# Kernel tuning notes

Hardware: AMD Instinct MI355X
Metric: run time of the kernel (lower is better)

The kernel has to match this reference:

```python
import math
import jax, jax.numpy as jnp
import numpy as np

H = 8  # num_heads

def _layernorm(x, scale, bias, eps=1e-5):
    m = x.mean(-1, keepdims=True)
    v = x.var(-1, keepdims=True)
    return (x - m) / jnp.sqrt(v + eps) * scale + bias

def setup_inputs() -> dict:
    key = jax.random.key(0)
    ks = jax.random.split(key, 12)
    B, C, P, D, G = 8, 32, 256, 256, 512
    n = jax.random.normal
    return {
        "qz": n(ks[0], (B, C, P, D), dtype=jnp.float32),
        "unary": n(ks[1], (B, C, P, D), dtype=jnp.float32),
        # per-sample condition-instantiated factors; scaled ~1/sqrt(D) so attn logits are sane
        "time_u": n(ks[2], (B, D, D), dtype=jnp.float32) * 0.06,
        "time_v": n(ks[3], (B, D, D), dtype=jnp.float32) * 0.06,
        "channel_u": n(ks[4], (B, D, D), dtype=jnp.float32) * 0.06,
        "channel_v": n(ks[5], (B, D, D), dtype=jnp.float32) * 0.06,
        "topic_binary": n(ks[6], (B, G, D), dtype=jnp.float32) * 0.02,
        "norm_scale": jnp.ones((D,), jnp.float32),
        "norm_bias": jnp.zeros((D,), jnp.float32),
        "gate_w": n(ks[7], (D, D), dtype=jnp.float32) * 0.02,
        "gate_b": jnp.zeros((D,), jnp.float32),
        "out_w1": n(ks[8], (D, D), dtype=jnp.float32) * 0.02,
        "out_b1": jnp.zeros((D,), jnp.float32),
        "out_w2": n(ks[9], (D, D), dtype=jnp.float32) * 0.02,
        "out_b2": jnp.zeros((D,), jnp.float32),
    }

def reference(qz, unary, time_u, time_v, channel_u, channel_v, topic_binary,
              norm_scale, norm_bias, gate_w, gate_b, out_w1, out_b1, out_w2, out_b2):
    B, C, P, D = qz.shape
    R = D // H
    inv_sqrt_r = 1.0 / math.sqrt(R)

    qz_n = _layernorm(qz, norm_scale, norm_bias)

    def heads(x, w):  # [B,C,P,D] x [B,D,D] -> [B,C,P,H,R]
        return jnp.einsum('bcpd,bod->bcpo', x, w).reshape(B, C, P, H, R)

    # --- time-factor message: attention over P within each (b, c, h) ---
    qu = heads(qz_n, time_u).transpose(0, 1, 3, 2, 4)   # [B,C,H,P,R]
    qv = heads(qz_n, time_v).transpose(0, 1, 3, 2, 4)
    attn_t = jax.nn.softmax(jnp.einsum('bchpr,bchqr->bchpq', qu, qv) * inv_sqrt_r, axis=-1)
    m_t = jnp.einsum('bchpq,bcqd->bchpd', attn_t, qz_n).mean(axis=2)  # [B,C,P,D]

    # --- channel-factor message: attention over C within each (b, p, h) ---
    qu = heads(qz_n, channel_u).transpose(0, 2, 3, 1, 4)  # [B,P,H,C,R]
    qv = heads(qz_n, channel_v).transpose(0, 2, 3, 1, 4)
    attn_c = jax.nn.softmax(jnp.einsum('bphcr,bphfr->bphcf', qu, qv) * inv_sqrt_r, axis=-1)
    qzp = qz_n.transpose(0, 2, 1, 3)                      # [B,P,C,D]
    m_c = jnp.einsum('bphcf,bpfd->bphcd', attn_c, qzp).mean(axis=2).transpose(0, 2, 1, 3)

    # --- topic-modeling binary factor with AbsNormalize (relu + L1-normalize) ---
    qg = jax.nn.relu(jnp.einsum('bcpd,bgd->bcpg', qz_n, topic_binary))
    qg = qg / jnp.maximum(qg.sum(axis=-1, keepdims=True), 1e-6)
    m_g = jnp.einsum('bcpg,bgd->bcpd', qg, topic_binary)

    # --- gated residual update ---
    gate = jax.nn.sigmoid(qz @ gate_w.T + gate_b)
    qz2 = gate * qz + (1.0 - gate) * (unary + m_t + m_c + m_g)

    # --- output MLP with shared LayerNorm ---
    h = _layernorm(qz2, norm_scale, norm_bias)
    h = jax.nn.gelu(h @ out_w1.T + out_b1, approximate=False) @ out_w2.T + out_b2
    return qz2 + h
```

## Files before the change

### kernel.cpp

```cpp
#include <hip/hip_runtime.h>
#include <math.h>

namespace {

constexpr float INV_SQRT_R = 0.17677669529663689f;

typedef __attribute__((ext_vector_type(8))) __bf16 bf16x8;
typedef __attribute__((ext_vector_type(4))) float f32x4;

static __device__ __forceinline__ f32x4 MF(bf16x8 a, bf16x8 b, f32x4 c) {
    return __builtin_amdgcn_mfma_f32_16x16x32_bf16(a, b, c, 0, 0, 0);
}

__global__ __launch_bounds__(256) void cvt_kernel(
    const float* __restrict__ src, __bf16* __restrict__ dst, int n)
{
    int i = (blockIdx.x * 256 + threadIdx.x) * 4;
    if (i < n) {
        float4 v = *(const float4*)(src + i);
        dst[i + 0] = (__bf16)v.x; dst[i + 1] = (__bf16)v.y;
        dst[i + 2] = (__bf16)v.z; dst[i + 3] = (__bf16)v.w;
    }
}

__global__ __launch_bounds__(256) void cvt2_kernel(
    const float* __restrict__ src, __bf16* __restrict__ dst, int n,
    int dstChunk, int dstOff)
{
    int i = (blockIdx.x * 256 + threadIdx.x) * 4;
    if (i < n) {
        float4 v = *(const float4*)(src + i);
        int o = (i >> 16) * dstChunk + dstOff + (i & 65535);
        dst[o + 0] = (__bf16)v.x; dst[o + 1] = (__bf16)v.y;
        dst[o + 2] = (__bf16)v.z; dst[o + 3] = (__bf16)v.w;
    }
}

__global__ __launch_bounds__(256) void ln_kernel(
    const float* __restrict__ x, const float* __restrict__ sc,
    const float* __restrict__ bi, __bf16* __restrict__ y)
{
    const size_t row = blockIdx.x;
    const int t = threadIdx.x;
    const float v = x[row * 256 + t];
    float s = v, s2 = v * v;
    #pragma unroll
    for (int o = 32; o > 0; o >>= 1) {
        s  += __shfl_xor(s, o);
        s2 += __shfl_xor(s2, o);
    }
    __shared__ float ps[4], ps2[4];
    if ((t & 63) == 0) { ps[t >> 6] = s; ps2[t >> 6] = s2; }
    __syncthreads();
    const float S  = ps[0] + ps[1] + ps[2] + ps[3];
    const float S2 = ps2[0] + ps2[1] + ps2[2] + ps2[3];
    const float mean = S * (1.0f / 256.0f);
    const float var  = S2 * (1.0f / 256.0f) - mean * mean;
    const float inv  = 1.0f / sqrtf(var + 1e-5f);
    y[row * 256 + t] = (__bf16)((v - mean) * inv * sc[t] + bi[t]);
}

__global__ __launch_bounds__(256) void tpose_bf_kernel(
    const __bf16* __restrict__ src, __bf16* __restrict__ dst, int R, int C)
{
    const size_t bz = blockIdx.z;
    src += bz * (size_t)R * C;
    dst += bz * (size_t)R * C;
    __shared__ __bf16 tile[32][34];
    const int r0 = blockIdx.x * 32, c0 = blockIdx.y * 32;
    const int tx = threadIdx.x & 31, ty = threadIdx.x >> 5;
    #pragma unroll
    for (int i = 0; i < 32; i += 8)
        tile[ty + i][tx] = src[(size_t)(r0 + ty + i) * C + c0 + tx];
    __syncthreads();
    #pragma unroll
    for (int i = 0; i < 32; i += 8)
        dst[(size_t)(c0 + ty + i) * R + r0 + tx] = tile[tx][ty + i];
}

__global__ __launch_bounds__(256) void tpose_cvt_kernel(
    const float* __restrict__ src, __bf16* __restrict__ dst, int R, int C)
{
    const size_t bz = blockIdx.z;
    src += bz * (size_t)R * C;
    dst += bz * (size_t)R * C;
    __shared__ __bf16 tile[32][34];
    const int r0 = blockIdx.x * 32, c0 = blockIdx.y * 32;
    const int tx = threadIdx.x & 31, ty = threadIdx.x >> 5;
    #pragma unroll
    for (int i = 0; i < 32; i += 8)
        tile[ty + i][tx] = (__bf16)src[(size_t)(r0 + ty + i) * C + c0 + tx];
    __syncthreads();
    #pragma unroll
    for (int i = 0; i < 32; i += 8)
        dst[(size_t)(c0 + ty + i) * R + r0 + tx] = tile[tx][ty + i];
}

__global__ __launch_bounds__(256) void mgemm_kernel(
    const __bf16* __restrict__ A, const __bf16* __restrict__ Bm, __bf16* __restrict__ Cout,
    int K, size_t aStride, size_t bStride,
    size_t s_b, size_t s_c, size_t s_p, size_t s_w, size_t s_h)
{
    const int bb = blockIdx.z;
    const int m0 = blockIdx.x * 64;
    const int n0 = blockIdx.y * 256;
    const __bf16* Ab = A + (size_t)bb * aStride;
    const __bf16* Bb = Bm + (size_t)bb * bStride;
    __shared__ __align__(16) __bf16 As[64][40];
    __shared__ __align__(16) __bf16 Bs[256][40];
    const int t = threadIdx.x;
    const int lane = t & 63;
    const int wid = t >> 6;
    const int l15 = lane & 15, lg = lane >> 4;

    f32x4 acc[4][4] = {};

    for (int k0 = 0; k0 < K; k0 += 32) {
        {
            const int row = t >> 2, k8 = (t & 3) << 3;
            *(bf16x8*)&As[row][k8] = *(const bf16x8*)(Ab + (size_t)(m0 + row) * K + k0 + k8);
        }
        #pragma unroll
        for (int s = 0; s < 4; ++s) {
            const int slot = s * 256 + t;
            const int row = slot >> 2, k8 = (slot & 3) << 3;
            *(bf16x8*)&Bs[row][k8] = *(const bf16x8*)(Bb + (size_t)(n0 + row) * K + k0 + k8);
        }
        __syncthreads();
        bf16x8 af[4], bfr[4];
        #pragma unroll
        for (int i = 0; i < 4; ++i)
            af[i] = *(const bf16x8*)&As[i * 16 + l15][lg * 8];
        #pragma unroll
        for (int j = 0; j < 4; ++j)
            bfr[j] = *(const bf16x8*)&Bs[wid * 64 + j * 16 + l15][lg * 8];
        #pragma unroll
        for (int i = 0; i < 4; ++i)
            #pragma unroll
            for (int j = 0; j < 4; ++j)
                acc[i][j] = MF(af[i], bfr[j], acc[i][j]);
        __syncthreads();
    }

    #pragma unroll
    for (int j = 0; j < 4; ++j) {
        const int n = n0 + wid * 64 + j * 16 + l15;
        const size_t offn = (size_t)(n >> 8) * s_w + (size_t)((n >> 5) & 7) * s_h + (n & 31);
        #pragma unroll
        for (int i = 0; i < 4; ++i) {
            #pragma unroll
            for (int r = 0; r < 4; ++r) {
                const int m = m0 + i * 16 + lg * 4 + r;
                const size_t off = (size_t)bb * s_b + (size_t)(m >> 8) * s_c
                                 + (size_t)(m & 255) * s_p + offn;
                Cout[off] = (__bf16)acc[i][j][r];
            }
        }
    }
}

__global__ __launch_bounds__(256) void time_attn_mt_kernel(
    const __bf16* __restrict__ qu, const __bf16* __restrict__ qv,
    const __bf16* __restrict__ qznT, __bf16* __restrict__ m_t)
{
    const int bc = blockIdx.x;
    const int p0 = blockIdx.y * 64;
    const __bf16* quB = qu + (size_t)bc * 65536;
    const __bf16* qvB = qv + (size_t)bc * 65536;
    const __bf16* BT  = qznT + (size_t)bc * 65536;
    __shared__ __align__(16) __bf16 R1[27136];
    __bf16* Us  = R1;
    __bf16* Vs  = R1 + 2560;
    __bf16* aL  = R1;
    __bf16* Bs2 = R1 + 16896;
    const int t = threadIdx.x;
    const int lane = t & 63;
    const int wid = t >> 6;
    const int l15 = lane & 15, lg = lane >> 4;

    f32x4 acc[16] = {};

    for (int h = 0; h < 8; ++h) {
        const __bf16* quH = quB + h * 8192;
        const __bf16* qvH = qvB + h * 8192;
        __syncthreads();
        {
            const int row = t >> 2, k8 = (t & 3) << 3;
            *(bf16x8*)&Us[row * 40 + k8] = *(const bf16x8*)(quH + (size_t)(p0 + row) * 32 + k8);
        }
        #pragma unroll
        for (int i = 0; i < 4; ++i) {
            const int slot = i * 256 + t;
            const int row = slot >> 2, k8 = (slot & 3) << 3;
            *(bf16x8*)&Vs[row * 40 + k8] = *(const bf16x8*)(qvH + (size_t)row * 32 + k8);
        }
        __syncthreads();

        f32x4 s[16];
        bf16x8 a = *(const bf16x8*)&Us[(wid * 16 + l15) * 40 + lg * 8];
        #pragma unroll
        for (int j = 0; j < 16; ++j) {
            bf16x8 bfr = *(const bf16x8*)&Vs[(j * 16 + l15) * 40 + lg * 8];
            s[j] = MF(a, bfr, (f32x4){0.f, 0.f, 0.f, 0.f});
        }

        #pragma unroll
        for (int r = 0; r < 4; ++r) {
            float e[16];
            float sum = 0.0f;
            #pragma unroll
            for (int j = 0; j < 16; ++j) {
                e[j] = __expf(s[j][r] * INV_SQRT_R);
                sum += e[j];
            }
            sum += __shfl_xor(sum, 1);
            sum += __shfl_xor(sum, 2);
            sum += __shfl_xor(sum, 4);
            sum += __shfl_xor(sum, 8);
            const float inv = 0.125f / sum;
            #pragma unroll
            for (int j = 0; j < 16; ++j) acc[j][r] += e[j] * inv;
        }
    }

    __syncthreads();
    #pragma unroll
    for (int r = 0; r < 4; ++r) {
        const int row = wid * 16 + lg * 4 + r;
        #pragma unroll
        for (int j = 0; j < 16; ++j)
            aL[row * 264 + j * 16 + l15] = (__bf16)acc[j][r];
    }
    __syncthreads();

    f32x4 acc2[4][4] = {};
    for (int k0 = 0; k0 < 256; k0 += 32) {
        #pragma unroll
        for (int s = 0; s < 4; ++s) {
            const int slot = s * 256 + t;
            const int row = slot >> 2, k8 = (slot & 3) << 3;
            *(bf16x8*)&Bs2[row * 40 + k8] = *(const bf16x8*)(BT + (size_t)row * 256 + k0 + k8);
        }
        __syncthreads();
        bf16x8 af[4], bfr[4];
        #pragma unroll
        for (int i = 0; i < 4; ++i)
            af[i] = *(const bf16x8*)&aL[(i * 16 + l15) * 264 + k0 + lg * 8];
        #pragma unroll
        for (int j = 0; j < 4; ++j)
            bfr[j] = *(const bf16x8*)&Bs2[(wid * 64 + j * 16 + l15) * 40 + lg * 8];
        #pragma unroll
        for (int i = 0; i < 4; ++i)
            #pragma unroll
            for (int j = 0; j < 4; ++j)
                acc2[i][j] = MF(af[i], bfr[j], acc2[i][j]);
        __syncthreads();
    }
    #pragma unroll
    for (int i = 0; i < 4; ++i)
        #pragma unroll
        for (int j = 0; j < 4; ++j) {
            const int d = wid * 64 + j * 16 + l15;
            #pragma unroll
            for (int r = 0; r < 4; ++r) {
                const int p = p0 + i * 16 + lg * 4 + r;
                m_t[(size_t)bc * 65536 + (size_t)p * 256 + d] = (__bf16)acc2[i][j][r];
            }
        }
}

__global__ __launch_bounds__(256) void chan_fused_kernel(
    const __bf16* __restrict__ quc, const __bf16* __restrict__ qvc,
    const __bf16* __restrict__ qzn, __bf16* __restrict__ m_c)
{
    const int bp = blockIdx.x;
    const int b = bp >> 8, p = bp & 255;
    const __bf16* quB = quc + (size_t)bp * 8192;
    const __bf16* qvB = qvc + (size_t)bp * 8192;
    __shared__ __align__(16) __bf16 QU[20480];
    __shared__ float ab[32 * 33];
    __bf16* qus = QU;
    __bf16* qvs = QU + 10240;
    const int t = threadIdx.x;
    #pragma unroll
    for (int i = 0; i < 4; ++i) {
        int fi = i * 256 + t;
        int e = fi << 3;
        int h = e >> 10, cc = (e >> 5) & 31, r = e & 31;
        int base = (h * 32 + cc) * 40 + r;
        *(bf16x8*)&qus[base] = *(const bf16x8*)(quB + e);
        *(bf16x8*)&qvs[base] = *(const bf16x8*)(qvB + e);
    }
    __syncthreads();
    const int c = t >> 3, j = t & 7;
    float acc[4] = {0.f, 0.f, 0.f, 0.f};
    for (int h = 0; h < 8; ++h) {
        float qur[32];
        #pragma unroll
        for (int u = 0; u < 4; ++u) {
            bf16x8 q8 = *(const bf16x8*)&qus[(h * 32 + c) * 40 + u * 8];
            #pragma unroll
            for (int e2 = 0; e2 < 8; ++e2) qur[u * 8 + e2] = (float)q8[e2];
        }
        float s[4];
        #pragma unroll
        for (int jj = 0; jj < 4; ++jj) {
            int f = j * 4 + jj;
            float a = 0.f;
            #pragma unroll
            for (int u = 0; u < 4; ++u) {
                bf16x8 v8 = *(const bf16x8*)&qvs[(h * 32 + f) * 40 + u * 8];
                #pragma unroll
                for (int e2 = 0; e2 < 8; ++e2) a += qur[u * 8 + e2] * (float)v8[e2];
            }
            s[jj] = a * INV_SQRT_R;
        }
        float mx = fmaxf(fmaxf(s[0], s[1]), fmaxf(s[2], s[3]));
        mx = fmaxf(mx, __shfl_xor(mx, 1));
        mx = fmaxf(mx, __shfl_xor(mx, 2));
        mx = fmaxf(mx, __shfl_xor(mx, 4));
        float e0x = __expf(s[0] - mx), e1x = __expf(s[1] - mx);
        float e2x = __expf(s[2] - mx), e3x = __expf(s[3] - mx);
        float sum = e0x + e1x + e2x + e3x;
        sum += __shfl_xor(sum, 1);
        sum += __shfl_xor(sum, 2);
        sum += __shfl_xor(sum, 4);
        float inv = 0.125f / sum;
        acc[0] += e0x * inv; acc[1] += e1x * inv; acc[2] += e2x * inv; acc[3] += e3x * inv;
    }
    #pragma unroll
    for (int jj = 0; jj < 4; ++jj) ab[c * 33 + j * 4 + jj] = acc[jj];
    __syncthreads();
    float* bt = (float*)QU;
    #pragma unroll 4
    for (int f = 0; f < 32; ++f)
        bt[f * 256 + t] = (float)qzn[((size_t)(b * 32 + f) * 256 + p) * 256 + t];
    __syncthreads();
    for (int c2 = 0; c2 < 32; c2 += 2) {
        float a0 = 0.f, a1 = 0.f;
        #pragma unroll
        for (int f = 0; f < 32; ++f) {
            float v = bt[f * 256 + t];
            a0 += ab[c2 * 33 + f] * v;
            a1 += ab[(c2 + 1) * 33 + f] * v;
        }
        size_t off = ((size_t)(b * 32 + c2) * 256 + p) * 256 + t;
        m_c[off] = (__bf16)a0;
        m_c[off + 65536] = (__bf16)a1;
    }
}

__global__ __launch_bounds__(256, 2) void topic_fused_kernel(
    const __bf16* __restrict__ qzn, const __bf16* __restrict__ topicb,
    const __bf16* __restrict__ topicTb, __bf16* __restrict__ m_g)
{
    const int bb = blockIdx.z;
    const int m0 = blockIdx.x * 32;
    const __bf16* Ab = qzn + (size_t)bb * 2097152;
    const __bf16* B1 = topicb + (size_t)bb * 131072;
    const __bf16* B2 = topicTb + (size_t)bb * 131072;
    __shared__ __align__(16) __bf16 As[32][40];
    __shared__ __align__(16) __bf16 Bs[512][40];
    __shared__ __align__(16) __bf16 Ps[32][520];
    __shared__ float rsInv[32];
    const int t = threadIdx.x;
    const int lane = t & 63, wid = t >> 6;
    const int l15 = lane & 15, lg = lane >> 4;

    f32x4 acc[2][8] = {};
    for (int k0 = 0; k0 < 256; k0 += 32) {
        if (t < 128) {
            const int row = t >> 2, k8 = (t & 3) << 3;
            *(bf16x8*)&As[row][k8] = *(const bf16x8*)(Ab + (size_t)(m0 + row) * 256 + k0 + k8);
        }
        #pragma unroll
        for (int s = 0; s < 8; ++s) {
            const int slot = s * 256 + t;
            const int row = slot >> 2, k8 = (slot & 3) << 3;
            *(bf16x8*)&Bs[row][k8] = *(const bf16x8*)(B1 + (size_t)row * 256 + k0 + k8);
        }
        __syncthreads();
        bf16x8 af0 = *(const bf16x8*)&As[l15][lg * 8];
        bf16x8 af1 = *(const bf16x8*)&As[16 + l15][lg * 8];
        #pragma unroll
        for (int j = 0; j < 8; ++j) {
            bf16x8 b8 = *(const bf16x8*)&Bs[wid * 128 + j * 16 + l15][lg * 8];
            acc[0][j] = MF(af0, b8, acc[0][j]);
            acc[1][j] = MF(af1, b8, acc[1][j]);
        }
        __syncthreads();
    }
    #pragma unroll
    for (int i = 0; i < 2; ++i)
        #pragma unroll
        for (int j = 0; j < 8; ++j) {
            const int n = wid * 128 + j * 16 + l15;
            #pragma unroll
            for (int r = 0; r < 4; ++r)
                Ps[i * 16 + lg * 4 + r][n] = (__bf16)fmaxf(acc[i][j][r], 0.0f);
        }
    __syncthreads();
    {
        const int row = t >> 3, seg = t & 7;
        float s = 0.0f;
        #pragma unroll
        for (int u = 0; u < 8; ++u) {
            bf16x8 v = *(const bf16x8*)&Ps[row][seg * 64 + u * 8];
            #pragma unroll
            for (int e = 0; e < 8; ++e) s += (float)v[e];
        }
        s += __shfl_xor(s, 1);
        s += __shfl_xor(s, 2);
        s += __shfl_xor(s, 4);
        if (seg == 0) rsInv[row] = 1.0f / fmaxf(s, 1e-6f);
    }
    __syncthreads();
    f32x4 acc2[2][4] = {};
    for (int k0 = 0; k0 < 512; k0 += 32) {
        #pragma unroll
        for (int s = 0; s < 4; ++s) {
            const int slot = s * 256 + t;
            const int row = slot >> 2, k8 = (slot & 3) << 3;
            *(bf16x8*)&Bs[row][k8] = *(const bf16x8*)(B2 + (size_t)row * 512 + k0 + k8);
        }
        __syncthreads();
        bf16x8 af0 = *(const bf16x8*)&Ps[l15][k0 + lg * 8];
        bf16x8 af1 = *(const bf16x8*)&Ps[16 + l15][k0 + lg * 8];
        #pragma unroll
        for (int j = 0; j < 4; ++j) {
            bf16x8 b8 = *(const bf16x8*)&Bs[wid * 64 + j * 16 + l15][lg * 8];
            acc2[0][j] = MF(af0, b8, acc2[0][j]);
            acc2[1][j] = MF(af1, b8, acc2[1][j]);
        }
        __syncthreads();
    }
    #pragma unroll
    for (int i = 0; i < 2; ++i)
        #pragma unroll
        for (int j = 0; j < 4; ++j) {
            const int n = wid * 64 + j * 16 + l15;
            #pragma unroll
            for (int r = 0; r < 4; ++r) {
                const int ml = i * 16 + lg * 4 + r;
                m_g[(size_t)bb * 2097152 + (size_t)(m0 + ml) * 256 + n]
                    = (__bf16)(acc2[i][j][r] * rsInv[ml]);
            }
        }
}

__global__ __launch_bounds__(256, 2) void mega_kernel(
    const float* __restrict__ qz, const float* __restrict__ unary,
    const __bf16* __restrict__ m_t, const __bf16* __restrict__ m_c,
    const __bf16* __restrict__ m_g,
    const __bf16* __restrict__ gwb, const float* __restrict__ gate_b,
    const __bf16* __restrict__ w1b, const float* __restrict__ b1,
    const __bf16* __restrict__ w2b, const float* __restrict__ b2,
    const float* __restrict__ nsc, const float* __restrict__ nbi,
    float* __restrict__ outp)
{
    const int m0 = blockIdx.x * 64;
    __shared__ __align__(16) __bf16 Bs[256][40];
    __shared__ __align__(16) __bf16 hL[64][264];
    __shared__ float lnp[64][4][2];
    const int t = threadIdx.x;
    const int lane = t & 63, wid = t >> 6;
    const int l15 = lane & 15, lg = lane >> 4;

    #pragma unroll
    for (int s = 0; s < 8; ++s) {
        const int slot = s * 256 + t;
        const int row = slot >> 5;
        const int k8 = (slot & 31) << 3;
        const float* src = qz + (size_t)(m0 + row) * 256 + k8;
        float4 v0 = *(const float4*)src;
        float4 v1 = *(const float4*)(src + 4);
        bf16x8 pk;
        pk[0] = (__bf16)v0.x; pk[1] = (__bf16)v0.y; pk[2] = (__bf16)v0.z; pk[3] = (__bf16)v0.w;
        pk[4] = (__bf16)v1.x; pk[5] = (__bf16)v1.y; pk[6] = (__bf16)v1.z; pk[7] = (__bf16)v1.w;
        *(bf16x8*)&hL[row][k8] = pk;
    }

    f32x4 acc[4][4] = {};
    for (int k0 = 0; k0 < 256; k0 += 32) {
        #pragma unroll
        for (int s = 0; s < 4; ++s) {
            const int slot = s * 256 + t;
            const int row = slot >> 2, k8 = (slot & 3) << 3;
            *(bf16x8*)&Bs[row][k8] = *(const bf16x8*)(gwb + (size_t)row * 256 + k0 + k8);
        }
        __syncthreads();
        bf16x8 af[4], bfr[4];
        #pragma unroll
        for (int i = 0; i < 4; ++i) af[i] = *(const bf16x8*)&hL[i * 16 + l15][k0 + lg * 8];
        #pragma unroll
        for (int j = 0; j < 4; ++j) bfr[j] = *(const bf16x8*)&Bs[wid * 64 + j * 16 + l15][lg * 8];
        #pragma unroll
        for (int i = 0; i < 4; ++i)
            #pragma unroll
            for (int j = 0; j < 4; ++j)
                acc[i][j] = MF(af[i], bfr[j], acc[i][j]);
        __syncthreads();
    }

    f32x4 z2[4][4];
    #pragma unroll
    for (int i = 0; i < 4; ++i) {
        #pragma unroll
        for (int r = 0; r < 4; ++r) {
            const int rr = i * 16 + lg * 4 + r;
            float s = 0.0f, s2 = 0.0f;
            #pragma unroll
            for (int j = 0; j < 4; ++j) {
                const int n = wid * 64 + j * 16 + l15;
                const size_t off = (size_t)(m0 + rr) * 256 + n;
                float g = 1.0f / (1.0f + __expf(-(acc[i][j][r] + gate_b[n])));
                float rest = unary[off] + (float)m_t[off] + (float)m_c[off] + (float)m_g[off];
                float v = g * (float)hL[rr][n] + (1.0f - g) * rest;
                z2[i][j][r] = v;
                s += v; s2 += v * v;
            }
            s  += __shfl_xor(s, 1);  s  += __shfl_xor(s, 2);
            s  += __shfl_xor(s, 4);  s  += __shfl_xor(s, 8);
            s2 += __shfl_xor(s2, 1); s2 += __shfl_xor(s2, 2);
            s2 += __shfl_xor(s2, 4); s2 += __shfl_xor(s2, 8);
            if (l15 == 0) {
                lnp[rr][wid][0] = s;
                lnp[rr][wid][1] = s2;
            }
        }
    }
    __syncthreads();
    #pragma unroll
    for (int i = 0; i < 4; ++i) {
        #pragma unroll
        for (int r = 0; r < 4; ++r) {
            const int rr = i * 16 + lg * 4 + r;
            float S  = lnp[rr][0][0] + lnp[rr][1][0] + lnp[rr][2][0] + lnp[rr][3][0];
            float S2 = lnp[rr][0][1] + lnp[rr][1][1] + lnp[rr][2][1] + lnp[rr][3][1];
            float mean = S * (1.0f / 256.0f);
            float var  = S2 * (1.0f / 256.0f) - mean * mean;
            float inv  = 1.0f / sqrtf(var + 1e-5f);
            #pragma unroll
            for (int j = 0; j < 4; ++j) {
                const int n = wid * 64 + j * 16 + l15;
                hL[rr][n] = (__bf16)((z2[i][j][r] - mean) * inv * nsc[n] + nbi[n]);
            }
        }
    }
    __syncthreads();

    f32x4 acc2[4][4] = {};
    for (int k0 = 0; k0 < 256; k0 += 32) {
        #pragma unroll
        for (int s = 0; s < 4; ++s) {
            const int slot = s * 256 + t;
            const int row = slot >> 2, k8 = (slot & 3) << 3;
            *(bf16x8*)&Bs[row][k8] = *(const bf16x8*)(w1b + (size_t)row * 256 + k0 + k8);
        }
        __syncthreads();
        bf16x8 af[4], bfr[4];
        #pragma unroll
        for (int i = 0; i < 4; ++i) af[i] = *(const bf16x8*)&hL[i * 16 + l15][k0 + lg * 8];
        #pragma unroll
        for (int j = 0; j < 4; ++j) bfr[j] = *(const bf16x8*)&Bs[wid * 64 + j * 16 + l15][lg * 8];
        #pragma unroll
        for (int i = 0; i < 4; ++i)
            #pragma unroll
            for (int j = 0; j < 4; ++j)
                acc2[i][j] = MF(af[i], bfr[j], acc2[i][j]);
        __syncthreads();
    }
    #pragma unroll
    for (int i = 0; i < 4; ++i)
        #pragma unroll
        for (int j = 0; j < 4; ++j) {
            const int n = wid * 64 + j * 16 + l15;
            const float bn = b1[n];
            #pragma unroll
            for (int r = 0; r < 4; ++r) {
                float x = acc2[i][j][r] + bn;
                hL[i * 16 + lg * 4 + r][n] = (__bf16)(0.5f * x * (1.0f + erff(x * 0.7071067811865475f)));
            }
        }
    __syncthreads();

    f32x4 acc3[4][4] = {};
    for (int k0 = 0; k0 < 256; k0 += 32) {
        #pragma unroll
        for (int s = 0; s < 4; ++s) {
            const int slot = s * 256 + t;
            const int row = slot >> 2, k8 = (slot & 3) << 3;
            *(bf16x8*)&Bs[row][k8] = *(const bf16x8*)(w2b + (size_t)row * 256 + k0 + k8);
        }
        __syncthreads();
        bf16x8 af[4], bfr[4];
        #pragma unroll
        for (int i = 0; i < 4; ++i) af[i] = *(const bf16x8*)&hL[i * 16 + l15][k0 + lg * 8];
        #pragma unroll
        for (int j = 0; j < 4; ++j) bfr[j] = *(const bf16x8*)&Bs[wid * 64 + j * 16 + l15][lg * 8];
        #pragma unroll
        for (int i = 0; i < 4; ++i)
            #pragma unroll
            for (int j = 0; j < 4; ++j)
                acc3[i][j] = MF(af[i], bfr[j], acc3[i][j]);
        __syncthreads();
    }
    #pragma unroll
    for (int i = 0; i < 4; ++i)
        #pragma unroll
        for (int j = 0; j < 4; ++j) {
            const int n = wid * 64 + j * 16 + l15;
            const float bn = b2[n];
            #pragma unroll
            for (int r = 0; r < 4; ++r) {
                const size_t off = (size_t)(m0 + i * 16 + lg * 4 + r) * 256 + n;
                outp[off] = z2[i][j][r] + acc3[i][j][r] + bn;
            }
        }
}

}

extern "C" void kernel_launch(void* const* d_in, const int* in_sizes, int n_in,
                              void* d_out, int out_size, void* d_ws, size_t ws_size,
                              hipStream_t stream)
{
    (void)in_sizes; (void)n_in; (void)out_size; (void)ws_size;
    const float* qz     = (const float*)d_in[0];
    const float* unary  = (const float*)d_in[1];
    const float* time_u = (const float*)d_in[2];
    const float* time_v = (const float*)d_in[3];
    const float* chan_u = (const float*)d_in[4];
    const float* chan_v = (const float*)d_in[5];
    const float* topic  = (const float*)d_in[6];
    const float* nsc    = (const float*)d_in[7];
    const float* nbi    = (const float*)d_in[8];
    const float* gate_w = (const float*)d_in[9];
    const float* gate_b = (const float*)d_in[10];
    const float* w1     = (const float*)d_in[11];
    const float* b1     = (const float*)d_in[12];
    const float* w2     = (const float*)d_in[13];
    const float* b2     = (const float*)d_in[14];

    char* base = (char*)d_ws;
    __bf16* qzn_b  = (__bf16*)base;
    __bf16* pool   = (__bf16*)(base + (32ull << 20));
    __bf16* wtime  = pool;
    __bf16* wchan  = pool + 1048576;
    __bf16* topicb = pool + 2097152;
    __bf16* topicTb= pool + 3145728;
    __bf16* gwb    = pool + 4194304;
    __bf16* w1b    = pool + 4259840;
    __bf16* w2b    = pool + 4325376;
    __bf16* Blo    = (__bf16*)(base + (64ull << 20));
    __bf16* Bhi    = (__bf16*)(base + (96ull << 20));
    __bf16* qu_t   = Blo;
    __bf16* qv_t   = Bhi;
    __bf16* qu_c   = Blo;
    __bf16* qv_c   = Bhi;
    __bf16* m_g    = Blo;
    __bf16* qznT   = (__bf16*)(base + (128ull << 20));
    __bf16* m_c    = qznT;
    __bf16* m_t    = (__bf16*)(base + (160ull << 20));
    float*  OUTF   = (float*)d_out;

    dim3 blk(256);

    cvt2_kernel<<<512, blk, 0, stream>>>(time_u, wtime, 524288, 131072, 0);
    cvt2_kernel<<<512, blk, 0, stream>>>(time_v, wtime, 524288, 131072, 65536);
    cvt2_kernel<<<512, blk, 0, stream>>>(chan_u, wchan, 524288, 131072, 0);
    cvt2_kernel<<<512, blk, 0, stream>>>(chan_v, wchan, 524288, 131072, 65536);
    cvt_kernel<<<1024, blk, 0, stream>>>(topic, topicb, 1048576);
    tpose_cvt_kernel<<<dim3(16, 8, 8), blk, 0, stream>>>(topic, topicTb, 512, 256);
    cvt_kernel<<<64, blk, 0, stream>>>(gate_w, gwb, 65536);
    cvt_kernel<<<64, blk, 0, stream>>>(w1, w1b, 65536);
    cvt_kernel<<<64, blk, 0, stream>>>(w2, w2b, 65536);

    ln_kernel<<<65536, blk, 0, stream>>>(qz, nsc, nbi, qzn_b);
    tpose_bf_kernel<<<dim3(8, 8, 256), blk, 0, stream>>>(qzn_b, qznT, 256, 256);

    mgemm_kernel<<<dim3(128, 2, 8), blk, 0, stream>>>(
        qzn_b, wtime, qu_t, 256, 2097152, 131072,
        2097152, 65536, 32, 16777216, 8192);

    time_attn_mt_kernel<<<dim3(256, 4), blk, 0, stream>>>(qu_t, qv_t, qznT, m_t);

    mgemm_kernel<<<dim3(128, 2, 8), blk, 0, stream>>>(
        qzn_b, wchan, qu_c, 256, 2097152, 131072,
        2097152, 32, 8192, 16777216, 1024);

    chan_fused_kernel<<<2048, blk, 0, stream>>>(qu_c, qv_c, qzn_b, m_c);

    topic_fused_kernel<<<dim3(256, 1, 8), blk, 0, stream>>>(qzn_b, topicb, topicTb, m_g);

    mega_kernel<<<1024, blk, 0, stream>>>(
        qz, unary, m_t, m_c, m_g,
        gwb, gate_b, w1b, b1, w2b, b2, nsc, nbi, OUTF);
}
```

Baseline: 540.7 us.

## Load GEMM B operands directly from global memory, drop LDS staging and syncs

Across the projection GEMM, time attention, topic and mega kernels, the B-operand (weights / transposed activations) is now read straight from global memory into MFMA fragments instead of being staged through shared memory every K-step. The A tile is loaded into LDS once for the full K, which removes the per-iteration barriers. The smaller LDS footprint allows higher occupancy hints in launch_bounds. The cost is more uncoalesced-ish 16-byte global loads that depend on L1/L2 reuse, since B rows are re-read by every block.

```diff
diff --git a/kernel.cpp b/kernel.cpp
--- a/kernel.cpp
+++ b/kernel.cpp
@@ -96,50 +96,45 @@
         dst[(size_t)(c0 + ty + i) * R + r0 + tx] = tile[tx][ty + i];
 }
 
-__global__ __launch_bounds__(256) void mgemm_kernel(
+__global__ __launch_bounds__(256, 4) void mgemm_kernel(
     const __bf16* __restrict__ A, const __bf16* __restrict__ Bm, __bf16* __restrict__ Cout,
-    int K, size_t aStride, size_t bStride,
+    size_t aStride, size_t bStride,
     size_t s_b, size_t s_c, size_t s_p, size_t s_w, size_t s_h)
 {
     const int bb = blockIdx.z;
     const int m0 = blockIdx.x * 64;
     const int n0 = blockIdx.y * 256;
     const __bf16* Ab = A + (size_t)bb * aStride;
-    const __bf16* Bb = Bm + (size_t)bb * bStride;
-    __shared__ __align__(16) __bf16 As[64][40];
-    __shared__ __align__(16) __bf16 Bs[256][40];
+    const __bf16* Bb = Bm + (size_t)bb * bStride + (size_t)n0 * 256;
+    __shared__ __align__(16) __bf16 As[64][264];
     const int t = threadIdx.x;
     const int lane = t & 63;
     const int wid = t >> 6;
     const int l15 = lane & 15, lg = lane >> 4;
 
+    #pragma unroll
+    for (int s = 0; s < 8; ++s) {
+        const int slot = s * 256 + t;
+        const int row = slot >> 5, k8 = (slot & 31) << 3;
+        *(bf16x8*)&As[row][k8] = *(const bf16x8*)(Ab + (size_t)(m0 + row) * 256 + k8);
+    }
+    __syncthreads();
+
     f32x4 acc[4][4] = {};
-
-    for (int k0 = 0; k0 < K; k0 += 32) {
-        {
-            const int row = t >> 2, k8 = (t & 3) << 3;
-            *(bf16x8*)&As[row][k8] = *(const bf16x8*)(Ab + (size_t)(m0 + row) * K + k0 + k8);
-        }
-        #pragma unroll
-        for (int s = 0; s < 4; ++s) {
-            const int slot = s * 256 + t;
-            const int row = slot >> 2, k8 = (slot & 3) << 3;
-            *(bf16x8*)&Bs[row][k8] = *(const bf16x8*)(Bb + (size_t)(n0 + row) * K + k0 + k8);
-        }
-        __syncthreads();
+    #pragma unroll
+    for (int k0 = 0; k0 < 256; k0 += 32) {
         bf16x8 af[4], bfr[4];
         #pragma unroll
         for (int i = 0; i < 4; ++i)
-            af[i] = *(const bf16x8*)&As[i * 16 + l15][lg * 8];
+            af[i] = *(const bf16x8*)&As[i * 16 + l15][k0 + lg * 8];
         #pragma unroll
         for (int j = 0; j < 4; ++j)
-            bfr[j] = *(const bf16x8*)&Bs[wid * 64 + j * 16 + l15][lg * 8];
+            bfr[j] = *(const bf16x8*)(Bb + (size_t)(wid * 64 + j * 16 + l15) * 256 + k0 + lg * 8);
         #pragma unroll
         for (int i = 0; i < 4; ++i)
             #pragma unroll
             for (int j = 0; j < 4; ++j)
                 acc[i][j] = MF(af[i], bfr[j], acc[i][j]);
-        __syncthreads();
     }
 
     #pragma unroll
@@ -159,7 +154,7 @@
     }
 }
 
-__global__ __launch_bounds__(256) void time_attn_mt_kernel(
+__global__ __launch_bounds__(256, 3) void time_attn_mt_kernel(
     const __bf16* __restrict__ qu, const __bf16* __restrict__ qv,
     const __bf16* __restrict__ qznT, __bf16* __restrict__ m_t)
 {
@@ -168,11 +163,10 @@
     const __bf16* quB = qu + (size_t)bc * 65536;
     const __bf16* qvB = qv + (size_t)bc * 65536;
     const __bf16* BT  = qznT + (size_t)bc * 65536;
-    __shared__ __align__(16) __bf16 R1[27136];
+    __shared__ __align__(16) __bf16 R1[16896];
     __bf16* Us  = R1;
     __bf16* Vs  = R1 + 2560;
     __bf16* aL  = R1;
-    __bf16* Bs2 = R1 + 16896;
     const int t = threadIdx.x;
     const int lane = t & 63;
     const int wid = t >> 6;
@@ -234,27 +228,20 @@
     __syncthreads();
 
     f32x4 acc2[4][4] = {};
+    #pragma unroll
     for (int k0 = 0; k0 < 256; k0 += 32) {
-        #pragma unroll
-        for (int s = 0; s < 4; ++s) {
-            const int slot = s * 256 + t;
-            const int row = slot >> 2, k8 = (slot & 3) << 3;
-            *(bf16x8*)&Bs2[row * 40 + k8] = *(const bf16x8*)(BT + (size_t)row * 256 + k0 + k8);
-        }
-        __syncthreads();
         bf16x8 af[4], bfr[4];
         #pragma unroll
         for (int i = 0; i < 4; ++i)
             af[i] = *(const bf16x8*)&aL[(i * 16 + l15) * 264 + k0 + lg * 8];
         #pragma unroll
         for (int j = 0; j < 4; ++j)
-            bfr[j] = *(const bf16x8*)&Bs2[(wid * 64 + j * 16 + l15) * 40 + lg * 8];
+            bfr[j] = *(const bf16x8*)(BT + (size_t)(wid * 64 + j * 16 + l15) * 256 + k0 + lg * 8);
         #pragma unroll
         for (int i = 0; i < 4; ++i)
             #pragma unroll
             for (int j = 0; j < 4; ++j)
                 acc2[i][j] = MF(af[i], bfr[j], acc2[i][j]);
-        __syncthreads();
     }
     #pragma unroll
     for (int i = 0; i < 4; ++i)
@@ -350,7 +337,7 @@
     }
 }
 
-__global__ __launch_bounds__(256, 2) void topic_fused_kernel(
+__global__ __launch_bounds__(256, 3) void topic_fused_kernel(
     const __bf16* __restrict__ qzn, const __bf16* __restrict__ topicb,
     const __bf16* __restrict__ topicTb, __bf16* __restrict__ m_g)
 {
@@ -359,36 +346,32 @@
     const __bf16* Ab = qzn + (size_t)bb * 2097152;
     const __bf16* B1 = topicb + (size_t)bb * 131072;
     const __bf16* B2 = topicTb + (size_t)bb * 131072;
-    __shared__ __align__(16) __bf16 As[32][40];
-    __shared__ __align__(16) __bf16 Bs[512][40];
+    __shared__ __align__(16) __bf16 As[32][264];
     __shared__ __align__(16) __bf16 Ps[32][520];
     __shared__ float rsInv[32];
     const int t = threadIdx.x;
     const int lane = t & 63, wid = t >> 6;
     const int l15 = lane & 15, lg = lane >> 4;
 
+    #pragma unroll
+    for (int s = 0; s < 4; ++s) {
+        const int slot = s * 256 + t;
+        const int row = slot >> 5, k8 = (slot & 31) << 3;
+        *(bf16x8*)&As[row][k8] = *(const bf16x8*)(Ab + (size_t)(m0 + row) * 256 + k8);
+    }
+    __syncthreads();
+
     f32x4 acc[2][8] = {};
+    #pragma unroll
     for (int k0 = 0; k0 < 256; k0 += 32) {
-        if (t < 128) {
-            const int row = t >> 2, k8 = (t & 3) << 3;
-            *(bf16x8*)&As[row][k8] = *(const bf16x8*)(Ab + (size_t)(m0 + row) * 256 + k0 + k8);
-        }
-        #pragma unroll
-        for (int s = 0; s < 8; ++s) {
-            const int slot = s * 256 + t;
-            const int row = slot >> 2, k8 = (slot & 3) << 3;
-            *(bf16x8*)&Bs[row][k8] = *(const bf16x8*)(B1 + (size_t)row * 256 + k0 + k8);
-        }
-        __syncthreads();
-        bf16x8 af0 = *(const bf16x8*)&As[l15][lg * 8];
-        bf16x8 af1 = *(const bf16x8*)&As[16 + l15][lg * 8];
+        bf16x8 af0 = *(const bf16x8*)&As[l15][k0 + lg * 8];
+        bf16x8 af1 = *(const bf16x8*)&As[16 + l15][k0 + lg * 8];
         #pragma unroll
         for (int j = 0; j < 8; ++j) {
-            bf16x8 b8 = *(const bf16x8*)&Bs[wid * 128 + j * 16 + l15][lg * 8];
+            bf16x8 b8 = *(const bf16x8*)(B1 + (size_t)(wid * 128 + j * 16 + l15) * 256 + k0 + lg * 8);
             acc[0][j] = MF(af0, b8, acc[0][j]);
             acc[1][j] = MF(af1, b8, acc[1][j]);
         }
-        __syncthreads();
     }
     #pragma unroll
     for (int i = 0; i < 2; ++i)
@@ -416,23 +399,16 @@
     }
     __syncthreads();
     f32x4 acc2[2][4] = {};
+    #pragma unroll
     for (int k0 = 0; k0 < 512; k0 += 32) {
-        #pragma unroll
-        for (int s = 0; s < 4; ++s) {
-            const int slot = s * 256 + t;
-            const int row = slot >> 2, k8 = (slot & 3) << 3;
-            *(bf16x8*)&Bs[row][k8] = *(const bf16x8*)(B2 + (size_t)row * 512 + k0 + k8);
-        }
-        __syncthreads();
         bf16x8 af0 = *(const bf16x8*)&Ps[l15][k0 + lg * 8];
         bf16x8 af1 = *(const bf16x8*)&Ps[16 + l15][k0 + lg * 8];
         #pragma unroll
         for (int j = 0; j < 4; ++j) {
-            bf16x8 b8 = *(const bf16x8*)&Bs[wid * 64 + j * 16 + l15][lg * 8];
+            bf16x8 b8 = *(const bf16x8*)(B2 + (size_t)(wid * 64 + j * 16 + l15) * 512 + k0 + lg * 8);
             acc2[0][j] = MF(af0, b8, acc2[0][j]);
             acc2[1][j] = MF(af1, b8, acc2[1][j]);
         }
-        __syncthreads();
     }
     #pragma unroll
     for (int i = 0; i < 2; ++i)
@@ -448,7 +424,7 @@
         }
 }
 
-__global__ __launch_bounds__(256, 2) void mega_kernel(
+__global__ __launch_bounds__(256, 3) void mega_kernel(
     const float* __restrict__ qz, const float* __restrict__ unary,
     const __bf16* __restrict__ m_t, const __bf16* __restrict__ m_c,
     const __bf16* __restrict__ m_g,
@@ -459,7 +435,6 @@
     float* __restrict__ outp)
 {
     const int m0 = blockIdx.x * 64;
-    __shared__ __align__(16) __bf16 Bs[256][40];
     __shared__ __align__(16) __bf16 hL[64][264];
     __shared__ float lnp[64][4][2];
     const int t = threadIdx.x;
@@ -479,27 +454,22 @@
         pk[4] = (__bf16)v1.x; pk[5] = (__bf16)v1.y; pk[6] = (__bf16)v1.z; pk[7] = (__bf16)v1.w;
         *(bf16x8*)&hL[row][k8] = pk;
     }
+    __syncthreads();
 
     f32x4 acc[4][4] = {};
+    #pragma unroll
     for (int k0 = 0; k0 < 256; k0 += 32) {
-        #pragma unroll
-        for (int s = 0; s < 4; ++s) {
-            const int slot = s * 256 + t;
-            const int row = slot >> 2, k8 = (slot & 3) << 3;
-            *(bf16x8*)&Bs[row][k8] = *(const bf16x8*)(gwb + (size_t)row * 256 + k0 + k8);
-        }
-        __syncthreads();
         bf16x8 af[4], bfr[4];
         #pragma unroll
         for (int i = 0; i < 4; ++i) af[i] = *(const bf16x8*)&hL[i * 16 + l15][k0 + lg * 8];
         #pragma unroll
-        for (int j = 0; j < 4; ++j) bfr[j] = *(const bf16x8*)&Bs[wid * 64 + j * 16 + l15][lg * 8];
+        for (int j = 0; j < 4; ++j)
+            bfr[j] = *(const bf16x8*)(gwb + (size_t)(wid * 64 + j * 16 + l15) * 256 + k0 + lg * 8);
         #pragma unroll
         for (int i = 0; i < 4; ++i)
             #pragma unroll
             for (int j = 0; j < 4; ++j)
                 acc[i][j] = MF(af[i], bfr[j], acc[i][j]);
-        __syncthreads();
     }
 
     f32x4 z2[4][4];
@@ -550,26 +520,21 @@
     __syncthreads();
 
     f32x4 acc2[4][4] = {};
+    #pragma unroll
     for (int k0 = 0; k0 < 256; k0 += 32) {
-        #pragma unroll
-        for (int s = 0; s < 4; ++s) {
-            const int slot = s * 256 + t;
-            const int row = slot >> 2, k8 = (slot & 3) << 3;
-            *(bf16x8*)&Bs[row][k8] = *(const bf16x8*)(w1b + (size_t)row * 256 + k0 + k8);
-        }
-        __syncthreads();
         bf16x8 af[4], bfr[4];
         #pragma unroll
         for (int i = 0; i < 4; ++i) af[i] = *(const bf16x8*)&hL[i * 16 + l15][k0 + lg * 8];
         #pragma unroll
-        for (int j = 0; j < 4; ++j) bfr[j] = *(const bf16x8*)&Bs[wid * 64 + j * 16 + l15][lg * 8];
+        for (int j = 0; j < 4; ++j)
+            bfr[j] = *(const bf16x8*)(w1b + (size_t)(wid * 64 + j * 16 + l15) * 256 + k0 + lg * 8);
         #pragma unroll
         for (int i = 0; i < 4; ++i)
             #pragma unroll
             for (int j = 0; j < 4; ++j)
                 acc2[i][j] = MF(af[i], bfr[j], acc2[i][j]);
-        __syncthreads();
-    }
+    }
+    __syncthreads();
     #pragma unroll
     for (int i = 0; i < 4; ++i)
         #pragma unroll
@@ -585,25 +550,19 @@
     __syncthreads();
 
     f32x4 acc3[4][4] = {};
+    #pragma unroll
     for (int k0 = 0; k0 < 256; k0 += 32) {
-        #pragma unroll
-        for (int s = 0; s < 4; ++s) {
-            const int slot = s * 256 + t;
-            const int row = slot >> 2, k8 = (slot & 3) << 3;
-            *(bf16x8*)&Bs[row][k8] = *(const bf16x8*)(w2b + (size_t)row * 256 + k0 + k8);
-        }
-        __syncthreads();
         bf16x8 af[4], bfr[4];
         #pragma unroll
         for (int i = 0; i < 4; ++i) af[i] = *(const bf16x8*)&hL[i * 16 + l15][k0 + lg * 8];
         #pragma unroll
-        for (int j = 0; j < 4; ++j) bfr[j] = *(const bf16x8*)&Bs[wid * 64 + j * 16 + l15][lg * 8];
+        for (int j = 0; j < 4; ++j)
+            bfr[j] = *(const bf16x8*)(w2b + (size_t)(wid * 64 + j * 16 + l15) * 256 + k0 + lg * 8);
         #pragma unroll
         for (int i = 0; i < 4; ++i)
             #pragma unroll
             for (int j = 0; j < 4; ++j)
                 acc3[i][j] = MF(af[i], bfr[j], acc3[i][j]);
-        __syncthreads();
     }
     #pragma unroll
     for (int i = 0; i < 4; ++i)
@@ -680,13 +639,13 @@
     tpose_bf_kernel<<<dim3(8, 8, 256), blk, 0, stream>>>(qzn_b, qznT, 256, 256);
 
     mgemm_kernel<<<dim3(128, 2, 8), blk, 0, stream>>>(
-        qzn_b, wtime, qu_t, 256, 2097152, 131072,
+        qzn_b, wtime, qu_t, 2097152, 131072,
         2097152, 65536, 32, 16777216, 8192);
 
     time_attn_mt_kernel<<<dim3(256, 4), blk, 0, stream>>>(qu_t, qv_t, qznT, m_t);
 
     mgemm_kernel<<<dim3(128, 2, 8), blk, 0, stream>>>(
-        qzn_b, wchan, qu_c, 256, 2097152, 131072,
+        qzn_b, wchan, qu_c, 2097152, 131072,
         2097152, 32, 8192, 16777216, 1024);
 
     chan_fused_kernel<<<2048, blk, 0, stream>>>(qu_c, qv_c, qzn_b, m_c);
```

Result: slower. 639.3 us (+18.2%).

## Remap block indices so batch varies fastest across XCDs, raise occupancy

Applied to the files above, without the earlier changes.

Flattens grids for the GEMM, time-attention, channel and topic kernels and remaps block ids so consecutive blocks map to different batch/bc groups. Given MI355X's round-robin dispatch of workgroups across XCDs, the intent appears to be keeping each batch's weights and data in one XCD's L2. The channel kernel now preloads its qzn column into registers before the attention phase instead of staging it through shared memory, removing a barrier and LDS traffic. The mega kernel reuses the Bs buffer for its LayerNorm partial sums to save LDS, and it and the channel kernel get occupancy hints of 3 blocks per CU, which risks register spills.

```diff
diff --git a/kernel.cpp b/kernel.cpp
--- a/kernel.cpp
+++ b/kernel.cpp
@@ -101,9 +101,11 @@
     int K, size_t aStride, size_t bStride,
     size_t s_b, size_t s_c, size_t s_p, size_t s_w, size_t s_h)
 {
-    const int bb = blockIdx.z;
-    const int m0 = blockIdx.x * 64;
-    const int n0 = blockIdx.y * 256;
+    const int bid = blockIdx.x;
+    const int bb = bid & 7;
+    const int rest = bid >> 3;
+    const int n0 = (rest & 1) * 256;
+    const int m0 = (rest >> 1) * 64;
     const __bf16* Ab = A + (size_t)bb * aStride;
     const __bf16* Bb = Bm + (size_t)bb * bStride;
     __shared__ __align__(16) __bf16 As[64][40];
@@ -163,8 +165,10 @@
     const __bf16* __restrict__ qu, const __bf16* __restrict__ qv,
     const __bf16* __restrict__ qznT, __bf16* __restrict__ m_t)
 {
-    const int bc = blockIdx.x;
-    const int p0 = blockIdx.y * 64;
+    const int bid = blockIdx.x;
+    const int jj0 = bid >> 3;
+    const int bc = (bid & 7) * 32 + (jj0 >> 2);
+    const int p0 = (jj0 & 3) * 64;
     const __bf16* quB = qu + (size_t)bc * 65536;
     const __bf16* qvB = qv + (size_t)bc * 65536;
     const __bf16* BT  = qznT + (size_t)bc * 65536;
@@ -269,12 +273,13 @@
         }
 }
 
-__global__ __launch_bounds__(256) void chan_fused_kernel(
+__global__ __launch_bounds__(256, 3) void chan_fused_kernel(
     const __bf16* __restrict__ quc, const __bf16* __restrict__ qvc,
     const __bf16* __restrict__ qzn, __bf16* __restrict__ m_c)
 {
-    const int bp = blockIdx.x;
-    const int b = bp >> 8, p = bp & 255;
+    const int bid = blockIdx.x;
+    const int b = bid & 7, p = bid >> 3;
+    const int bp = b * 256 + p;
     const __bf16* quB = quc + (size_t)bp * 8192;
     const __bf16* qvB = qvc + (size_t)bp * 8192;
     __shared__ __align__(16) __bf16 QU[20480];
@@ -282,6 +287,12 @@
     __bf16* qus = QU;
     __bf16* qvs = QU + 10240;
     const int t = threadIdx.x;
+
+    float btr[32];
+    #pragma unroll
+    for (int f = 0; f < 32; ++f)
+        btr[f] = (float)qzn[((size_t)(b * 32 + f) * 256 + p) * 256 + t];
+
     #pragma unroll
     for (int i = 0; i < 4; ++i) {
         int fi = i * 256 + t;
@@ -331,16 +342,12 @@
     #pragma unroll
     for (int jj = 0; jj < 4; ++jj) ab[c * 33 + j * 4 + jj] = acc[jj];
     __syncthreads();
-    float* bt = (float*)QU;
-    #pragma unroll 4
-    for (int f = 0; f < 32; ++f)
-        bt[f * 256 + t] = (float)qzn[((size_t)(b * 32 + f) * 256 + p) * 256 + t];
-    __syncthreads();
+    #pragma unroll 2
     for (int c2 = 0; c2 < 32; c2 += 2) {
         float a0 = 0.f, a1 = 0.f;
         #pragma unroll
         for (int f = 0; f < 32; ++f) {
-            float v = bt[f * 256 + t];
+            float v = btr[f];
             a0 += ab[c2 * 33 + f] * v;
             a1 += ab[(c2 + 1) * 33 + f] * v;
         }
@@ -354,8 +361,9 @@
     const __bf16* __restrict__ qzn, const __bf16* __restrict__ topicb,
     const __bf16* __restrict__ topicTb, __bf16* __restrict__ m_g)
 {
-    const int bb = blockIdx.z;
-    const int m0 = blockIdx.x * 32;
+    const int bid = blockIdx.x;
+    const int bb = bid & 7;
+    const int m0 = (bid >> 3) * 32;
     const __bf16* Ab = qzn + (size_t)bb * 2097152;
     const __bf16* B1 = topicb + (size_t)bb * 131072;
     const __bf16* B2 = topicTb + (size_t)bb * 131072;
@@ -448,7 +456,7 @@
         }
 }
 
-__global__ __launch_bounds__(256, 2) void mega_kernel(
+__global__ __launch_bounds__(256, 3) void mega_kernel(
     const float* __restrict__ qz, const float* __restrict__ unary,
     const __bf16* __restrict__ m_t, const __bf16* __restrict__ m_c,
     const __bf16* __restrict__ m_g,
@@ -461,7 +469,7 @@
     const int m0 = blockIdx.x * 64;
     __shared__ __align__(16) __bf16 Bs[256][40];
     __shared__ __align__(16) __bf16 hL[64][264];
-    __shared__ float lnp[64][4][2];
+    float* lnp = (float*)Bs;
     const int t = threadIdx.x;
     const int lane = t & 63, wid = t >> 6;
     const int l15 = lane & 15, lg = lane >> 4;
@@ -524,8 +532,8 @@
             s2 += __shfl_xor(s2, 1); s2 += __shfl_xor(s2, 2);
             s2 += __shfl_xor(s2, 4); s2 += __shfl_xor(s2, 8);
             if (l15 == 0) {
-                lnp[rr][wid][0] = s;
-                lnp[rr][wid][1] = s2;
+                lnp[rr * 8 + wid * 2 + 0] = s;
+                lnp[rr * 8 + wid * 2 + 1] = s2;
             }
         }
     }
@@ -535,8 +543,8 @@
         #pragma unroll
         for (int r = 0; r < 4; ++r) {
             const int rr = i * 16 + lg * 4 + r;
-            float S  = lnp[rr][0][0] + lnp[rr][1][0] + lnp[rr][2][0] + lnp[rr][3][0];
-            float S2 = lnp[rr][0][1] + lnp[rr][1][1] + lnp[rr][2][1] + lnp[rr][3][1];
+            float S  = lnp[rr * 8 + 0] + lnp[rr * 8 + 2] + lnp[rr * 8 + 4] + lnp[rr * 8 + 6];
+            float S2 = lnp[rr * 8 + 1] + lnp[rr * 8 + 3] + lnp[rr * 8 + 5] + lnp[rr * 8 + 7];
             float mean = S * (1.0f / 256.0f);
             float var  = S2 * (1.0f / 256.0f) - mean * mean;
             float inv  = 1.0f / sqrtf(var + 1e-5f);
@@ -679,19 +687,19 @@
     ln_kernel<<<65536, blk, 0, stream>>>(qz, nsc, nbi, qzn_b);
     tpose_bf_kernel<<<dim3(8, 8, 256), blk, 0, stream>>>(qzn_b, qznT, 256, 256);
 
-    mgemm_kernel<<<dim3(128, 2, 8), blk, 0, stream>>>(
+    mgemm_kernel<<<2048, blk, 0, stream>>>(
         qzn_b, wtime, qu_t, 256, 2097152, 131072,
         2097152, 65536, 32, 16777216, 8192);
 
-    time_attn_mt_kernel<<<dim3(256, 4), blk, 0, stream>>>(qu_t, qv_t, qznT, m_t);
-
-    mgemm_kernel<<<dim3(128, 2, 8), blk, 0, stream>>>(
+    time_attn_mt_kernel<<<1024, blk, 0, stream>>>(qu_t, qv_t, qznT, m_t);
+
+    mgemm_kernel<<<2048, blk, 0, stream>>>(
         qzn_b, wchan, qu_c, 256, 2097152, 131072,
         2097152, 32, 8192, 16777216, 1024);
 
     chan_fused_kernel<<<2048, blk, 0, stream>>>(qu_c, qv_c, qzn_b, m_c);
 
-    topic_fused_kernel<<<dim3(256, 1, 8), blk, 0, stream>>>(qzn_b, topicb, topicTb, m_g);
+    topic_fused_kernel<<<2048, blk, 0, stream>>>(qzn_b, topicb, topicTb, m_g);
 
     mega_kernel<<<1024, blk, 0, stream>>>(
         qz, unary, m_t, m_c, m_g,
```

Measured after the change: 575.5 us. 1.06x slower.
